# Kernel tuning notes

Hardware: AMD Instinct MI355X
Metric: run time of the kernel (lower is better)

## Reference

```python
import jax, jax.numpy as jnp
import numpy as np

N_SERIES = 32768
N_TIME = 512
SEAS = 24
MAX_NUM_SERIES = 32768
OUTPUT_SIZE = 7


def setup_inputs() -> dict:
    key = jax.random.key(0)
    k1, k2, k3, k4, k5 = jax.random.split(key, 5)
    # y must be strictly positive (divisions and logs of levels)
    y = jax.random.uniform(k1, (N_SERIES, N_TIME), jnp.float32) + 0.5
    idxs = jax.random.randint(k2, (N_SERIES,), 0, MAX_NUM_SERIES)
    lev_sms = jax.random.normal(k3, (MAX_NUM_SERIES, 1), jnp.float32) * 0.5
    seas_sms = jax.random.normal(k4, (MAX_NUM_SERIES, 1), jnp.float32) * 0.5
    init_seas = jax.random.normal(k5, (MAX_NUM_SERIES, SEAS), jnp.float32) * 0.1
    return {
        "y": y,
        "idxs": idxs,
        "lev_sms": lev_sms,
        "seas_sms": seas_sms,
        "init_seas": init_seas,
        "seasonality": SEAS,
        "output_size": OUTPUT_SIZE,
    }


def _es_forward(y, idxs, lev_sms_p, seas_sms_p, init_seas_p, seasonality, output_size):
    n_series, n_time = y.shape
    lev_sms = jax.nn.sigmoid(lev_sms_p[idxs, 0])          # (n,)
    # NOTE: faithful to original code, which (buggy or not) derives seas_sms
    # from self.lev_sms as well; seas_sms_p is an unused parameter.
    seas_sms = jax.nn.sigmoid(lev_sms_p[idxs, 0])         # (n,)
    init_seas = jnp.exp(init_seas_p[idxs, :])             # (n, seasonality)

    lev0 = y[:, 0] / init_seas[:, 0]                      # levels[:,0]

    # Ring-buffer formulation of the lag-`seasonality` recurrence:
    # original reads seasonalities[:, t] and writes seasonalities[:, t+seasonality];
    # both map to slot t % seasonality (read-before-write). Initial buffer slots
    # equal init_seas columns (slot 0 = init_seas[:,0], which also covers the
    # duplicated entry seasonalities[:, seasonality]).
    positions = jnp.arange(1, n_time) % seasonality       # (n_time-1,)
    y_steps = y[:, 1:].T                                  # (n_time-1, n)

    def step(carry, xs):
        lev_prev, buf = carry                             # (n,), (n, seasonality)
        y_t, pos = xs
        seas_t = buf[:, pos]
        newlev = lev_sms * (y_t / seas_t) + (1.0 - lev_sms) * lev_prev
        newseason = seas_sms * (y_t / newlev) + (1.0 - seas_sms) * seas_t
        log_diff = jnp.log(newlev) - jnp.log(lev_prev)
        buf = buf.at[:, pos].set(newseason)
        return (newlev, buf), (newlev, newseason, log_diff)

    _, (levs, seasons, logd) = jax.lax.scan(step, (lev0, init_seas), (y_steps, positions))

    levels = jnp.concatenate([lev0[:, None], levs.T], axis=1)              # (n, n_time)
    seasonalities = jnp.concatenate(
        [init_seas, init_seas[:, :1], seasons.T], axis=1                   # (n, seasonality+n_time)
    )
    log_diff_of_levels = logd.T                                            # (n, n_time-1)

    if output_size > seasonality:
        # faithful to original (which uses len(seasonalities) == n_series)
        start = seasonalities.shape[0] - seasonality
        end = start + output_size - seasonality
        seasonalities = jnp.concatenate([seasonalities, seasonalities[:, start:end]], axis=1)

    return levels, seasonalities, log_diff_of_levels


def reference(y, idxs, lev_sms, seas_sms, init_seas, seasonality, output_size):
    return _es_forward(y, idxs, lev_sms, seas_sms, init_seas, seasonality, output_size)
```

## Files before the change

### kernel.cpp

```cpp
#include <hip/hip_runtime.h>

#define NT 512
#define SEAS 24
constexpr int SEA_STRIDE = NT + SEAS;
constexpr int LOG_STRIDE = NT - 1;
constexpr float LN2 = 0.6931471805599453f;

__device__ __forceinline__ float frcp(float x)  { return __builtin_amdgcn_rcpf(x); }
__device__ __forceinline__ float flog2(float x) { return __builtin_amdgcn_logf(x); }

__global__ __launch_bounds__(64)
void es_fwd(const float* __restrict__ y, const int* __restrict__ idxs,
            const float* __restrict__ lev_sms_p, const float* __restrict__ init_seas_p,
            float* __restrict__ levels, float* __restrict__ seas, float* __restrict__ logd)
{
    const int s = blockIdx.x * 64 + threadIdx.x;
    const int idx = idxs[s];
    const float lsm = frcp(1.0f + __expf(-lev_sms_p[idx]));
    const float ssm = lsm;

    const float* __restrict__ yrow  = y      + (size_t)s * NT;
    float* __restrict__ levrow      = levels + (size_t)s * NT;
    float* __restrict__ searow      = seas   + (size_t)s * SEA_STRIDE;
    float* __restrict__ logrow      = logd   + (size_t)s * LOG_STRIDE;

    float buf[SEAS];
    {
        const float4* is4 = (const float4*)(init_seas_p + (size_t)idx * SEAS);
        #pragma unroll
        for (int g = 0; g < 6; ++g) {
            float4 v = is4[g];
            float a = __expf(v.x), b = __expf(v.y), c = __expf(v.z), d = __expf(v.w);
            buf[4*g+0]=a; buf[4*g+1]=b; buf[4*g+2]=c; buf[4*g+3]=d;
            float4 o; o.x=a; o.y=b; o.z=c; o.w=d;
            ((float4*)searow)[g] = o;
        }
    }

    const float4* y4 = (const float4*)yrow;
    float yv[24], yn[24];
    #pragma unroll
    for (int g = 0; g < 6; ++g) {
        float4 t = y4[g];
        yv[4*g]=t.x; yv[4*g+1]=t.y; yv[4*g+2]=t.z; yv[4*g+3]=t.w;
    }

    float lev, l2prev;
    float lvv[24], svv[24];

#define STEP(POS, KI, TI) do { \
        const float yt = yv[KI]; \
        const float st = buf[POS]; \
        const float nl = lev + lsm * (yt * frcp(st) - lev); \
        const float ns = st + ssm * (yt * frcp(nl) - st); \
        const float l2 = flog2(nl); \
        lvv[KI] = nl; svv[KI] = ns; \
        logrow[(TI)-1] = (l2 - l2prev) * LN2; \
        l2prev = l2; lev = nl; buf[POS] = ns; \
    } while (0)

#define STORE_BLOCK(TBASE) do { \
        float4* lp_ = (float4*)(levrow + (TBASE)); \
        float4* sp_ = (float4*)(searow + SEAS + (TBASE)); \
        _Pragma("unroll") \
        for (int g = 0; g < 6; ++g) { \
            float4 o; o.x=lvv[4*g]; o.y=lvv[4*g+1]; o.z=lvv[4*g+2]; o.w=lvv[4*g+3]; \
            lp_[g] = o; \
            float4 p; p.x=svv[4*g]; p.y=svv[4*g+1]; p.z=svv[4*g+2]; p.w=svv[4*g+3]; \
            sp_[g] = p; \
        } \
    } while (0)

    #pragma unroll
    for (int g = 0; g < 6; ++g) {
        float4 t = y4[6+g];
        yn[4*g]=t.x; yn[4*g+1]=t.y; yn[4*g+2]=t.z; yn[4*g+3]=t.w;
    }
    lev = yv[0] * frcp(buf[0]);
    l2prev = flog2(lev);
    lvv[0] = lev;
    svv[0] = buf[0];
    #pragma unroll
    for (int k = 1; k < 24; ++k) STEP(k, k, k);
    STORE_BLOCK(0);
    #pragma unroll
    for (int k = 0; k < 24; ++k) yv[k] = yn[k];

    for (int m = 1; m < 21; ++m) {
        if (m < 20) {
            #pragma unroll
            for (int g = 0; g < 6; ++g) {
                float4 t = y4[6*(m+1)+g];
                yn[4*g]=t.x; yn[4*g+1]=t.y; yn[4*g+2]=t.z; yn[4*g+3]=t.w;
            }
        } else {
            float4 t0 = y4[126];
            float4 t1 = y4[127];
            yn[0]=t0.x; yn[1]=t0.y; yn[2]=t0.z; yn[3]=t0.w;
            yn[4]=t1.x; yn[5]=t1.y; yn[6]=t1.z; yn[7]=t1.w;
        }
        const int tb = 24*m;
        #pragma unroll
        for (int k = 0; k < 24; ++k) STEP(k, k, tb + k);
        STORE_BLOCK(tb);
        #pragma unroll
        for (int k = 0; k < 24; ++k) yv[k] = yn[k];
    }

    {
        const int tb = 504;
        #pragma unroll
        for (int k = 0; k < 8; ++k) STEP(k, k, tb + k);
        float4* lp = (float4*)(levrow + tb);
        float4* sp = (float4*)(searow + SEAS + tb);
        #pragma unroll
        for (int g = 0; g < 2; ++g) {
            float4 o; o.x=lvv[4*g]; o.y=lvv[4*g+1]; o.z=lvv[4*g+2]; o.w=lvv[4*g+3];
            lp[g] = o;
            float4 p; p.x=svv[4*g]; p.y=svv[4*g+1]; p.z=svv[4*g+2]; p.w=svv[4*g+3];
            sp[g] = p;
        }
    }
#undef STEP
#undef STORE_BLOCK
}

extern "C" void kernel_launch(void* const* d_in, const int* in_sizes, int n_in,
                              void* d_out, int out_size, void* d_ws, size_t ws_size,
                              hipStream_t stream)
{
    const float* y        = (const float*)d_in[0];
    const int*   idxs     = (const int*)d_in[1];
    const float* lev_sms  = (const float*)d_in[2];
    const float* init_seas = (const float*)d_in[4];
    const int n_series = in_sizes[1];

    float* levels = (float*)d_out;
    float* seasv  = levels + (size_t)n_series * NT;
    float* logdv  = seasv  + (size_t)n_series * SEA_STRIDE;

    es_fwd<<<n_series / 64, 64, 0, stream>>>(y, idxs, lev_sms, init_seas,
                                             levels, seasv, logdv);
}
```

Baseline: 366.5 us.

## Stage y tiles through LDS with async global-to-LDS loads and transpose outputs

Replaces per-thread strided row reads and writes with a tiled scheme. Each 48-step tile of y for the 64 series is loaded with global_load_lds, one time column per lane, so global accesses coalesce across lanes. Results are buffered in padded LDS tiles and written back transposed, so consecutive lanes write consecutive time steps. Loading the next tile overlaps with flushing the current one. The cost is LDS capacity, fewer wide vector stores, and a single-wave block that relies on waitcnt without barriers, so LDS reuse between tiles needs careful ordering.

```diff
diff --git a/kernel.cpp b/kernel.cpp
--- a/kernel.cpp
+++ b/kernel.cpp
@@ -1,137 +1,141 @@
 #include <hip/hip_runtime.h>
 
 #define NT 512
-#define SEAS 24
-constexpr int SEA_STRIDE = NT + SEAS;
+#define SEASN 24
+#define TT 48
+
+constexpr int SEA_STRIDE = NT + SEASN;
 constexpr int LOG_STRIDE = NT - 1;
 constexpr float LN2 = 0.6931471805599453f;
 
 __device__ __forceinline__ float frcp(float x)  { return __builtin_amdgcn_rcpf(x); }
 __device__ __forceinline__ float flog2(float x) { return __builtin_amdgcn_logf(x); }
 
+__device__ __forceinline__ void gl_lds4(const float* g, float* lds) {
+    __builtin_amdgcn_global_load_lds(
+        (const __attribute__((address_space(1))) void*)g,
+        (__attribute__((address_space(3))) void*)lds, 4, 0, 0);
+}
+
+struct State { float lev, l2prev; };
+
+template<int T, bool FIRST>
+__device__ __forceinline__ void compute_tile(const float* __restrict__ ybuf,
+                                             float2* __restrict__ c2,
+                                             float* __restrict__ dtile,
+                                             int lane, float lsm,
+                                             float (&buf)[SEASN], State& st)
+{
+    #pragma unroll
+    for (int k = 0; k < T; ++k) {
+        const int pos = k % SEASN;
+        const float yt = ybuf[lane * 49 + k];
+        if (FIRST && k == 0) {
+            st.lev = yt * frcp(buf[0]);
+            st.l2prev = flog2(st.lev);
+            c2[lane] = make_float2(st.lev, buf[0]);
+        } else {
+            const float sv = buf[pos];
+            const float nl = st.lev + lsm * (yt * frcp(sv) - st.lev);
+            const float ns = sv + lsm * (yt * frcp(nl) - sv);
+            const float l2 = flog2(nl);
+            c2[k * 65 + lane] = make_float2(nl, ns);
+            dtile[k * 65 + lane] = (l2 - st.l2prev) * LN2;
+            st.l2prev = l2; st.lev = nl; buf[pos] = ns;
+        }
+    }
+}
+
+__device__ __forceinline__ void flush_tile(const float2* __restrict__ c2,
+                                           const float* __restrict__ dtile,
+                                           int lane, int sbase, int tbase, int T,
+                                           float* __restrict__ levels,
+                                           float* __restrict__ seasv,
+                                           float* __restrict__ logd)
+{
+    if (lane < T) {
+        #pragma unroll 16
+        for (int r = 0; r < 64; ++r) {
+            const size_t srow = (size_t)(sbase + r);
+            const float2 ls = c2[lane * 65 + r];
+            const float dv = dtile[lane * 65 + r];
+            levels[srow * NT + tbase + lane] = ls.x;
+            seasv[srow * SEA_STRIDE + SEASN + tbase + lane] = ls.y;
+            if (tbase + lane > 0)
+                logd[srow * LOG_STRIDE + tbase + lane - 1] = dv;
+        }
+    }
+}
+
 __global__ __launch_bounds__(64)
 void es_fwd(const float* __restrict__ y, const int* __restrict__ idxs,
             const float* __restrict__ lev_sms_p, const float* __restrict__ init_seas_p,
-            float* __restrict__ levels, float* __restrict__ seas, float* __restrict__ logd)
+            float* __restrict__ levels, float* __restrict__ seasv,
+            float* __restrict__ logd)
 {
-    const int s = blockIdx.x * 64 + threadIdx.x;
+    __shared__ float ybuf[64 * 49];
+    __shared__ __align__(16) float2 c2[TT * 65];
+    __shared__ float dtile[TT * 65];
+
+    const int lane = threadIdx.x;
+    const int sbase = blockIdx.x * 64;
+    const int s = sbase + lane;
     const int idx = idxs[s];
     const float lsm = frcp(1.0f + __expf(-lev_sms_p[idx]));
-    const float ssm = lsm;
 
-    const float* __restrict__ yrow  = y      + (size_t)s * NT;
-    float* __restrict__ levrow      = levels + (size_t)s * NT;
-    float* __restrict__ searow      = seas   + (size_t)s * SEA_STRIDE;
-    float* __restrict__ logrow      = logd   + (size_t)s * LOG_STRIDE;
-
-    float buf[SEAS];
+    float buf[SEASN];
     {
-        const float4* is4 = (const float4*)(init_seas_p + (size_t)idx * SEAS);
+        float* searow = seasv + (size_t)s * SEA_STRIDE;
+        const float4* is4 = (const float4*)(init_seas_p + (size_t)idx * SEASN);
         #pragma unroll
         for (int g = 0; g < 6; ++g) {
             float4 v = is4[g];
             float a = __expf(v.x), b = __expf(v.y), c = __expf(v.z), d = __expf(v.w);
-            buf[4*g+0]=a; buf[4*g+1]=b; buf[4*g+2]=c; buf[4*g+3]=d;
+            buf[4*g]=a; buf[4*g+1]=b; buf[4*g+2]=c; buf[4*g+3]=d;
             float4 o; o.x=a; o.y=b; o.z=c; o.w=d;
             ((float4*)searow)[g] = o;
         }
     }
 
-    const float4* y4 = (const float4*)yrow;
-    float yv[24], yn[24];
-    #pragma unroll
-    for (int g = 0; g < 6; ++g) {
-        float4 t = y4[g];
-        yv[4*g]=t.x; yv[4*g+1]=t.y; yv[4*g+2]=t.z; yv[4*g+3]=t.w;
+    const float* ysrc = y + (size_t)sbase * NT + lane;
+    auto stage = [&](int tbase, int cols) {
+        if (lane < cols) {
+            const float* g = ysrc + tbase;
+            #pragma unroll
+            for (int r = 0; r < 64; ++r)
+                gl_lds4(g + (size_t)r * NT, &ybuf[r * 49]);
+        }
+    };
+
+    State st;
+
+    stage(0, TT);
+    __builtin_amdgcn_s_waitcnt(0);
+    compute_tile<TT, true>(ybuf, c2, dtile, lane, lsm, buf, st);
+
+    stage(TT, TT);
+    flush_tile(c2, dtile, lane, sbase, 0, TT, levels, seasv, logd);
+    __builtin_amdgcn_s_waitcnt(0);
+
+    for (int m = 1; m <= 9; ++m) {
+        compute_tile<TT, false>(ybuf, c2, dtile, lane, lsm, buf, st);
+        if (m < 9) stage((m + 1) * TT, TT);
+        else       stage(480, 32);
+        flush_tile(c2, dtile, lane, sbase, m * TT, TT, levels, seasv, logd);
+        __builtin_amdgcn_s_waitcnt(0);
     }
 
-    float lev, l2prev;
-    float lvv[24], svv[24];
-
-#define STEP(POS, KI, TI) do { \
-        const float yt = yv[KI]; \
-        const float st = buf[POS]; \
-        const float nl = lev + lsm * (yt * frcp(st) - lev); \
-        const float ns = st + ssm * (yt * frcp(nl) - st); \
-        const float l2 = flog2(nl); \
-        lvv[KI] = nl; svv[KI] = ns; \
-        logrow[(TI)-1] = (l2 - l2prev) * LN2; \
-        l2prev = l2; lev = nl; buf[POS] = ns; \
-    } while (0)
-
-#define STORE_BLOCK(TBASE) do { \
-        float4* lp_ = (float4*)(levrow + (TBASE)); \
-        float4* sp_ = (float4*)(searow + SEAS + (TBASE)); \
-        _Pragma("unroll") \
-        for (int g = 0; g < 6; ++g) { \
-            float4 o; o.x=lvv[4*g]; o.y=lvv[4*g+1]; o.z=lvv[4*g+2]; o.w=lvv[4*g+3]; \
-            lp_[g] = o; \
-            float4 p; p.x=svv[4*g]; p.y=svv[4*g+1]; p.z=svv[4*g+2]; p.w=svv[4*g+3]; \
-            sp_[g] = p; \
-        } \
-    } while (0)
-
-    #pragma unroll
-    for (int g = 0; g < 6; ++g) {
-        float4 t = y4[6+g];
-        yn[4*g]=t.x; yn[4*g+1]=t.y; yn[4*g+2]=t.z; yn[4*g+3]=t.w;
-    }
-    lev = yv[0] * frcp(buf[0]);
-    l2prev = flog2(lev);
-    lvv[0] = lev;
-    svv[0] = buf[0];
-    #pragma unroll
-    for (int k = 1; k < 24; ++k) STEP(k, k, k);
-    STORE_BLOCK(0);
-    #pragma unroll
-    for (int k = 0; k < 24; ++k) yv[k] = yn[k];
-
-    for (int m = 1; m < 21; ++m) {
-        if (m < 20) {
-            #pragma unroll
-            for (int g = 0; g < 6; ++g) {
-                float4 t = y4[6*(m+1)+g];
-                yn[4*g]=t.x; yn[4*g+1]=t.y; yn[4*g+2]=t.z; yn[4*g+3]=t.w;
-            }
-        } else {
-            float4 t0 = y4[126];
-            float4 t1 = y4[127];
-            yn[0]=t0.x; yn[1]=t0.y; yn[2]=t0.z; yn[3]=t0.w;
-            yn[4]=t1.x; yn[5]=t1.y; yn[6]=t1.z; yn[7]=t1.w;
-        }
-        const int tb = 24*m;
-        #pragma unroll
-        for (int k = 0; k < 24; ++k) STEP(k, k, tb + k);
-        STORE_BLOCK(tb);
-        #pragma unroll
-        for (int k = 0; k < 24; ++k) yv[k] = yn[k];
-    }
-
-    {
-        const int tb = 504;
-        #pragma unroll
-        for (int k = 0; k < 8; ++k) STEP(k, k, tb + k);
-        float4* lp = (float4*)(levrow + tb);
-        float4* sp = (float4*)(searow + SEAS + tb);
-        #pragma unroll
-        for (int g = 0; g < 2; ++g) {
-            float4 o; o.x=lvv[4*g]; o.y=lvv[4*g+1]; o.z=lvv[4*g+2]; o.w=lvv[4*g+3];
-            lp[g] = o;
-            float4 p; p.x=svv[4*g]; p.y=svv[4*g+1]; p.z=svv[4*g+2]; p.w=svv[4*g+3];
-            sp[g] = p;
-        }
-    }
-#undef STEP
-#undef STORE_BLOCK
+    compute_tile<32, false>(ybuf, c2, dtile, lane, lsm, buf, st);
+    flush_tile(c2, dtile, lane, sbase, 480, 32, levels, seasv, logd);
 }
 
 extern "C" void kernel_launch(void* const* d_in, const int* in_sizes, int n_in,
                               void* d_out, int out_size, void* d_ws, size_t ws_size,
                               hipStream_t stream)
 {
-    const float* y        = (const float*)d_in[0];
-    const int*   idxs     = (const int*)d_in[1];
-    const float* lev_sms  = (const float*)d_in[2];
+    const float* y         = (const float*)d_in[0];
+    const int*   idxs      = (const int*)d_in[1];
+    const float* lev_sms   = (const float*)d_in[2];
     const float* init_seas = (const float*)d_in[4];
     const int n_series = in_sizes[1];
 
```

Result: faster. 346.8 us (-5.4%).
